# Kernel tuning notes

Hardware: AMD Instinct MI355X
Metric: run time of the kernel (lower is better)

## Reference

```python
import jax, jax.numpy as jnp
import numpy as np

N, E = 40000, 640000
IN_DIM, EDGE_DIM, HID = 128, 64, 128


def setup_inputs() -> dict:
    key = jax.random.key(0)
    ks = jax.random.split(key, 10)
    x = jax.random.normal(ks[0], (N, IN_DIM), dtype=jnp.float32)
    edge_index = jax.random.randint(ks[1], (2, E), 0, N, dtype=jnp.int64)
    edge_attr = jax.random.normal(ks[2], (E, EDGE_DIM), dtype=jnp.float32)
    # learned params (xavier-ish scaling)
    Wh_w = jax.random.normal(ks[3], (EDGE_DIM, HID), dtype=jnp.float32) / np.sqrt(EDGE_DIM)
    Wh_b = jnp.zeros((HID,), dtype=jnp.float32)
    Wn_w = jax.random.normal(ks[4], (2 * IN_DIM, HID), dtype=jnp.float32) / np.sqrt(2 * IN_DIM)
    Wn_b = jnp.zeros((HID,), dtype=jnp.float32)
    w_e = jax.random.normal(ks[5], (HID, 1), dtype=jnp.float32) / np.sqrt(HID)
    ft_w = jax.random.normal(ks[6], (IN_DIM, IN_DIM), dtype=jnp.float32) / np.sqrt(IN_DIM)
    ft_b = jnp.zeros((IN_DIM,), dtype=jnp.float32)
    return {"x": x, "edge_index": edge_index, "edge_attr": edge_attr,
            "Wh_w": Wh_w, "Wh_b": Wh_b, "Wn_w": Wn_w, "Wn_b": Wn_b,
            "w_e": w_e, "ft_w": ft_w, "ft_b": ft_b}


def reference(x, edge_index, edge_attr, Wh_w, Wh_b, Wn_w, Wn_b, w_e, ft_w, ft_b):
    src, dst = edge_index[0], edge_index[1]
    # gather endpoint features and run edge MLP: relu(W_h(e) + W_n([x_src; x_dst]))
    node_feat = jnp.concatenate([x[src], x[dst]], axis=1)          # [E, 2*in_dim]
    edge_h = edge_attr @ Wh_w + Wh_b                               # [E, hid]
    node_h = node_feat @ Wn_w + Wn_b                               # [E, hid]
    combined = jax.nn.relu(edge_h + node_h)
    scores = (combined @ w_e)[:, 0]                                # [E]
    alpha = jax.nn.softmax(scores, axis=0)                         # softmax over all edges
    # scatter-add weighted dst features into src nodes (same-type branch)
    local = jnp.zeros_like(x).at[src].add(-alpha[:, None] * x[dst])
    out = x + local
    out = out + out @ ft_w + ft_b
    return out
```

## Files before the change

### kernel.cpp

```cpp
#include <hip/hip_runtime.h>
#include <math.h>

#define N_NODES 40000
#define E_EDGES 640000
#define IN_DIM 128
#define EDGE_DIM 64
#define HID 128
#define EB 10000

typedef unsigned int u32;
typedef unsigned short u16;
typedef __attribute__((ext_vector_type(4))) float f32x4;
typedef __attribute__((ext_vector_type(8))) short bf16x8;

__device__ __forceinline__ float bf_lo(u32 d) { return __uint_as_float(d << 16); }
__device__ __forceinline__ float bf_hi(u32 d) { return __uint_as_float(d & 0xffff0000u); }
__device__ __forceinline__ u16 f2bf(float f) {
    u32 u = __float_as_uint(f);
    return (u16)((u + 0x7fffu + ((u >> 16) & 1u)) >> 16);
}


__global__ __launch_bounds__(256) void k_init(const float* __restrict__ x,
                                              u16* __restrict__ xb,
                                              u32* __restrict__ counts) {
    int i = blockIdx.x * 256 + threadIdx.x;
    xb[i] = f2bf(x[i]);
    if (i < N_NODES) counts[i] = 0;
}

__global__ __launch_bounds__(256) void k_trans(const float* __restrict__ Wh,
                                               u16* __restrict__ Whtb) {
    int i = blockIdx.x * 256 + threadIdx.x;
    int h = i >> 6;
    int k = i & 63;
    Whtb[i] = f2bf(Wh[k * HID + h]);
}

__global__ __launch_bounds__(256) void k_proj(const float* __restrict__ x,
                                              const float* __restrict__ Wn,
                                              const float* __restrict__ Whb,
                                              const float* __restrict__ Wnb,
                                              u16* __restrict__ P1b,
                                              u16* __restrict__ P2b) {
    __shared__ float xs[16][IN_DIM];
    const int rowBase = blockIdx.x * 16;

    const float4* xsrc = (const float4*)(x + (size_t)rowBase * IN_DIM);
    float4* xd = (float4*)&xs[0][0];
    for (int i = threadIdx.x; i < 16 * IN_DIM / 4; i += 256) xd[i] = xsrc[i];
    __syncthreads();

    const int h  = threadIdx.x & 127;
    const int rg = threadIdx.x >> 7;

    float acc1[8], acc2[8];
#pragma unroll
    for (int r = 0; r < 8; ++r) { acc1[r] = 0.f; acc2[r] = 0.f; }

    for (int k = 0; k < IN_DIM; ++k) {
        float wa = Wn[k * HID + h];
        float wb = Wn[(IN_DIM + k) * HID + h];
#pragma unroll
        for (int r = 0; r < 8; ++r) {
            float xv = xs[rg * 8 + r][k];
            acc1[r] += xv * wa;
            acc2[r] += xv * wb;
        }
    }
    const float bias = Whb[h] + Wnb[h];
#pragma unroll
    for (int r = 0; r < 8; ++r) {
        int row = rowBase + rg * 8 + r;
        P1b[(size_t)row * HID + h] = f2bf(acc1[r] + bias);
        P2b[(size_t)row * HID + h] = f2bf(acc2[r]);
    }
}

__global__ __launch_bounds__(256) void k_hist(const int* __restrict__ eidx,
                                              u32* __restrict__ counts) {
    int e = blockIdx.x * 256 + threadIdx.x;
    atomicAdd(&counts[eidx[e]], 1u);
}

__global__ __launch_bounds__(1024) void k_scan(const u32* __restrict__ counts,
                                               u32* __restrict__ off,
                                               u32* __restrict__ cur) {
    __shared__ u32 sums[1024];
    const int t = threadIdx.x;
    const int CH = 40;
    u32 local[CH];
    u32 s = 0;
    const int base = t * CH;
#pragma unroll
    for (int i = 0; i < CH; ++i) {
        int idx = base + i;
        u32 c = (idx < N_NODES) ? counts[idx] : 0u;
        local[i] = s;
        s += c;
    }
    sums[t] = s;
    __syncthreads();
    for (int o = 1; o < 1024; o <<= 1) {
        u32 v = (t >= o) ? sums[t - o] : 0u;
        __syncthreads();
        sums[t] += v;
        __syncthreads();
    }
    const u32 pre = sums[t] - s;
#pragma unroll
    for (int i = 0; i < CH; ++i) {
        int idx = base + i;
        if (idx < N_NODES) {
            u32 v = pre + local[i];
            off[idx] = v;
            cur[idx] = v;
        }
    }
    if (t == 1023) off[N_NODES] = sums[1023];
}

__global__ __launch_bounds__(256) void k_edge(const int* __restrict__ eidx,
                                              const float* __restrict__ ea,
                                              const u16* __restrict__ Whtb,
                                              const u16* __restrict__ P1b,
                                              const u16* __restrict__ P2b,
                                              const float* __restrict__ we,
                                              float* __restrict__ expS,
                                              float* __restrict__ partials) {
    __shared__ float Ps[64][132];
    __shared__ float wsumLds[4];
    const int e0 = blockIdx.x * 64;
    const int t = threadIdx.x;

    {
        const int m = t >> 2, c4 = t & 3;
        int src = eidx[e0 + m];
        int dst = eidx[E_EDGES + e0 + m];
        const uint4* p1 = (const uint4*)(P1b + (size_t)src * HID + c4 * 32);
        const uint4* p2 = (const uint4*)(P2b + (size_t)dst * HID + c4 * 32);
#pragma unroll
        for (int i = 0; i < 4; ++i) {
            uint4 ua = p1[i], ub = p2[i];
            u32 da[4] = {ua.x, ua.y, ua.z, ua.w};
            u32 db[4] = {ub.x, ub.y, ub.z, ub.w};
#pragma unroll
            for (int j = 0; j < 4; ++j) {
                Ps[m][c4 * 32 + i * 8 + 2 * j]     = bf_lo(da[j]) + bf_lo(db[j]);
                Ps[m][c4 * 32 + i * 8 + 2 * j + 1] = bf_hi(da[j]) + bf_hi(db[j]);
            }
        }
    }
    __syncthreads();

    const int w = t >> 6, lane = t & 63;
    const int mrow = lane & 15, quad = lane >> 4;
    const int mt = w;

    const float* arow = ea + (size_t)(e0 + mt * 16 + mrow) * EDGE_DIM + quad * 8;
    bf16x8 a0, a1;
#pragma unroll
    for (int ks = 0; ks < 2; ++ks) {
        float4 f0 = *(const float4*)(arow + ks * 32);
        float4 f1 = *(const float4*)(arow + ks * 32 + 4);
        bf16x8& af = ks ? a1 : a0;
        af[0] = (short)f2bf(f0.x); af[1] = (short)f2bf(f0.y);
        af[2] = (short)f2bf(f0.z); af[3] = (short)f2bf(f0.w);
        af[4] = (short)f2bf(f1.x); af[5] = (short)f2bf(f1.y);
        af[6] = (short)f2bf(f1.z); af[7] = (short)f2bf(f1.w);
    }

    float wsum[4] = {0.f, 0.f, 0.f, 0.f};
    const u16* bbase = Whtb + (size_t)mrow * EDGE_DIM + quad * 8;
#pragma unroll
    for (int nt = 0; nt < 8; ++nt) {
        const u16* bp = bbase + nt * 16 * EDGE_DIM;
        bf16x8 b0 = *(const bf16x8*)(bp);
        bf16x8 b1 = *(const bf16x8*)(bp + 32);
        f32x4 c = {0.f, 0.f, 0.f, 0.f};
        c = __builtin_amdgcn_mfma_f32_16x16x32_bf16(a0, b0, c, 0, 0, 0);
        c = __builtin_amdgcn_mfma_f32_16x16x32_bf16(a1, b1, c, 0, 0, 0);
        float wv = we[nt * 16 + mrow];
#pragma unroll
        for (int r = 0; r < 4; ++r) {
            float v = c[r] + Ps[mt * 16 + quad * 4 + r][nt * 16 + mrow];
            wsum[r] += fmaxf(v, 0.f) * wv;
        }
    }

#pragma unroll
    for (int off = 1; off < 16; off <<= 1) {
#pragma unroll
        for (int r = 0; r < 4; ++r) wsum[r] += __shfl_xor(wsum[r], off, 16);
    }
    float ex[4]; float s4 = 0.f;
#pragma unroll
    for (int r = 0; r < 4; ++r) { ex[r] = __expf(wsum[r]); s4 += ex[r]; }
    if (mrow == 0) {
#pragma unroll
        for (int r = 0; r < 4; ++r) expS[e0 + mt * 16 + quad * 4 + r] = ex[r];
    }
    s4 += __shfl_xor(s4, 16, 64);
    s4 += __shfl_xor(s4, 32, 64);
    if (lane == 0) wsumLds[w] = s4;
    __syncthreads();
    if (t == 0) partials[blockIdx.x] = wsumLds[0] + wsumLds[1] + wsumLds[2] + wsumLds[3];
}

__global__ __launch_bounds__(256) void k_sum(const float* __restrict__ partials,
                                             float* __restrict__ sumExp) {
    float s = 0.f;
    for (int i = threadIdx.x; i < EB; i += 256) s += partials[i];
#pragma unroll
    for (int off = 1; off < 64; off <<= 1) s += __shfl_xor(s, off, 64);
    __shared__ float ws4[4];
    if ((threadIdx.x & 63) == 0) ws4[threadIdx.x >> 6] = s;
    __syncthreads();
    if (threadIdx.x == 0) sumExp[0] = ws4[0] + ws4[1] + ws4[2] + ws4[3];
}

__global__ __launch_bounds__(256) void k_fill(const int* __restrict__ eidx,
                                              const float* __restrict__ expS,
                                              const float* __restrict__ sumExp,
                                              u32* __restrict__ cur,
                                              u32* __restrict__ sdst,
                                              float* __restrict__ sa) {
    const float invS = 1.0f / sumExp[0];
    int e = blockIdx.x * 256 + threadIdx.x;
    int src = eidx[e];
    int dst = eidx[E_EDGES + e];
    u32 pos = atomicAdd(&cur[src], 1u);
    sdst[pos] = (u32)dst;
    sa[pos]   = -expS[e] * invS;
}

__global__ __launch_bounds__(256) void k_accum(const u32* __restrict__ off,
                                               const u32* __restrict__ sdst,
                                               const float* __restrict__ sa,
                                               const u16* __restrict__ xb,
                                               float* __restrict__ out) {
    const int lane = threadIdx.x & 63;
    const int n = blockIdx.x * 4 + (threadIdx.x >> 6);
    const u32 o0 = off[n], o1 = off[n + 1];

    float acc0 = 0.f, acc1 = 0.f;
    for (u32 base = o0; base < o1; base += 64) {
        u32 j = base + (u32)lane;
        u32 dv = 0; float av = 0.f;
        if (j < o1) { dv = sdst[j]; av = sa[j]; }
        int cnt = (int)min(64u, o1 - base);
        for (int jj = 0; jj < cnt; ++jj) {
            u32 dst = __shfl(dv, jj, 64);
            float a = __shfl(av, jj, 64);
            u32 d = ((const u32*)(xb + (size_t)dst * IN_DIM))[lane];
            acc0 = fmaf(a, bf_lo(d), acc0);
            acc1 = fmaf(a, bf_hi(d), acc1);
        }
    }
    float* op = out + (size_t)n * IN_DIM + 2 * lane;
    op[0] = acc0;
    op[1] = acc1;
}

__global__ __launch_bounds__(256) void k_final(const float* __restrict__ x,
                                               const float* __restrict__ ft,
                                               const float* __restrict__ ftb,
                                               float* __restrict__ out) {
    __shared__ float ys[16][IN_DIM];
    const int rowBase = blockIdx.x * 16;

    const float4* xsrc = (const float4*)(x + (size_t)rowBase * IN_DIM);
    const float4* lsrc = (const float4*)(out + (size_t)rowBase * IN_DIM);
    float4* yd = (float4*)&ys[0][0];
    for (int i = threadIdx.x; i < 16 * IN_DIM / 4; i += 256) {
        float4 a = xsrc[i];
        float4 b = lsrc[i];
        a.x += b.x; a.y += b.y; a.z += b.z; a.w += b.w;
        yd[i] = a;
    }
    __syncthreads();

    const int h  = threadIdx.x & 127;
    const int rg = threadIdx.x >> 7;

    float acc[8];
#pragma unroll
    for (int r = 0; r < 8; ++r) acc[r] = 0.f;

    for (int k = 0; k < IN_DIM; ++k) {
        float w = ft[k * IN_DIM + h];
#pragma unroll
        for (int r = 0; r < 8; ++r) acc[r] += ys[rg * 8 + r][k] * w;
    }
    const float b = ftb[h];
#pragma unroll
    for (int r = 0; r < 8; ++r) {
        int row = rowBase + rg * 8 + r;
        out[(size_t)row * IN_DIM + h] = ys[rg * 8 + r][h] + acc[r] + b;
    }
}

extern "C" void kernel_launch(void* const* d_in, const int* in_sizes, int n_in,
                              void* d_out, int out_size, void* d_ws, size_t ws_size,
                              hipStream_t stream) {
    const float* x    = (const float*)d_in[0];
    const int*   eidx = (const int*)d_in[1];
    const float* ea   = (const float*)d_in[2];
    const float* Whw  = (const float*)d_in[3];
    const float* Whb  = (const float*)d_in[4];
    const float* Wnw  = (const float*)d_in[5];
    const float* Wnb  = (const float*)d_in[6];
    const float* we   = (const float*)d_in[7];
    const float* ftw  = (const float*)d_in[8];
    const float* ftb  = (const float*)d_in[9];
    float* out = (float*)d_out;

    u16*   P1b      = (u16*)d_ws;
    u16*   P2b      = P1b + (size_t)N_NODES * HID;
    u16*   xb       = P2b + (size_t)N_NODES * HID;
    u16*   Whtb     = xb + (size_t)N_NODES * IN_DIM;
    float* expS     = (float*)(Whtb + (size_t)EDGE_DIM * HID);
    float* partials = expS + (size_t)E_EDGES;
    float* sumExp   = partials + EB;
    u32*   counts   = (u32*)(sumExp + 1);
    u32*   off      = counts + N_NODES;
    u32*   cur      = off + N_NODES + 1;
    u32*   sdst     = cur + N_NODES;
    float* sa       = (float*)(sdst + E_EDGES);

    k_init <<<(N_NODES * IN_DIM) / 256, 256, 0, stream>>>(x, xb, counts);
    k_trans<<<(EDGE_DIM * HID) / 256, 256, 0, stream>>>(Whw, Whtb);
    k_proj <<<N_NODES / 16, 256, 0, stream>>>(x, Wnw, Whb, Wnb, P1b, P2b);
    k_hist <<<E_EDGES / 256, 256, 0, stream>>>(eidx, counts);
    k_scan <<<1, 1024, 0, stream>>>(counts, off, cur);
    k_edge <<<EB, 256, 0, stream>>>(eidx, ea, Whtb, P1b, P2b, we, expS, partials);
    k_sum  <<<1, 256, 0, stream>>>(partials, sumExp);
    k_fill <<<E_EDGES / 256, 256, 0, stream>>>(eidx, expS, sumExp, cur, sdst, sa);
    k_accum<<<N_NODES / 4, 256, 0, stream>>>(off, sdst, sa, xb, out);
    k_final<<<N_NODES / 16, 256, 0, stream>>>(x, ftw, ftb, out);
}
```

Baseline: 587.4 us.

## Move node projection and final transform GEMMs onto bf16 MFMA

```diff
diff --git a/kernel.cpp b/kernel.cpp
--- a/kernel.cpp
+++ b/kernel.cpp
@@ -19,6 +19,9 @@
     u32 u = __float_as_uint(f);
     return (u16)((u + 0x7fffu + ((u >> 16) & 1u)) >> 16);
 }
+__device__ __forceinline__ u32 pack_bf(float lo, float hi) {
+    return ((u32)f2bf(hi) << 16) | (u32)f2bf(lo);
+}
 
 
 __global__ __launch_bounds__(256) void k_init(const float* __restrict__ x,
@@ -29,51 +32,63 @@
     if (i < N_NODES) counts[i] = 0;
 }
 
-__global__ __launch_bounds__(256) void k_trans(const float* __restrict__ Wh,
-                                               u16* __restrict__ Whtb) {
+__global__ __launch_bounds__(256) void k_trans(const float* __restrict__ Whw,
+                                               const float* __restrict__ Wnw,
+                                               const float* __restrict__ ftw,
+                                               u16* __restrict__ Whtb,
+                                               u16* __restrict__ WnAT,
+                                               u16* __restrict__ WnBT,
+                                               u16* __restrict__ fttb) {
     int i = blockIdx.x * 256 + threadIdx.x;
-    int h = i >> 6;
-    int k = i & 63;
-    Whtb[i] = f2bf(Wh[k * HID + h]);
-}
-
-__global__ __launch_bounds__(256) void k_proj(const float* __restrict__ x,
-                                              const float* __restrict__ Wn,
+    if (i < 8192) {
+        int h = i >> 6, k = i & 63;
+        Whtb[i] = f2bf(Whw[k * HID + h]);
+    } else if (i < 24576) {
+        int j = i - 8192, h = j >> 7, k = j & 127;
+        WnAT[j] = f2bf(Wnw[k * HID + h]);
+    } else if (i < 40960) {
+        int j = i - 24576, h = j >> 7, k = j & 127;
+        WnBT[j] = f2bf(Wnw[(IN_DIM + k) * HID + h]);
+    } else {
+        int j = i - 40960, h = j >> 7, k = j & 127;
+        fttb[j] = f2bf(ftw[k * IN_DIM + h]);
+    }
+}
+
+__global__ __launch_bounds__(256) void k_proj(const u16* __restrict__ xb,
+                                              const u16* __restrict__ WnAT,
+                                              const u16* __restrict__ WnBT,
                                               const float* __restrict__ Whb,
                                               const float* __restrict__ Wnb,
                                               u16* __restrict__ P1b,
                                               u16* __restrict__ P2b) {
-    __shared__ float xs[16][IN_DIM];
-    const int rowBase = blockIdx.x * 16;
-
-    const float4* xsrc = (const float4*)(x + (size_t)rowBase * IN_DIM);
-    float4* xd = (float4*)&xs[0][0];
-    for (int i = threadIdx.x; i < 16 * IN_DIM / 4; i += 256) xd[i] = xsrc[i];
-    __syncthreads();
-
-    const int h  = threadIdx.x & 127;
-    const int rg = threadIdx.x >> 7;
-
-    float acc1[8], acc2[8];
-#pragma unroll
-    for (int r = 0; r < 8; ++r) { acc1[r] = 0.f; acc2[r] = 0.f; }
-
-    for (int k = 0; k < IN_DIM; ++k) {
-        float wa = Wn[k * HID + h];
-        float wb = Wn[(IN_DIM + k) * HID + h];
-#pragma unroll
-        for (int r = 0; r < 8; ++r) {
-            float xv = xs[rg * 8 + r][k];
-            acc1[r] += xv * wa;
-            acc2[r] += xv * wb;
-        }
-    }
-    const float bias = Whb[h] + Wnb[h];
-#pragma unroll
-    for (int r = 0; r < 8; ++r) {
-        int row = rowBase + rg * 8 + r;
-        P1b[(size_t)row * HID + h] = f2bf(acc1[r] + bias);
-        P2b[(size_t)row * HID + h] = f2bf(acc2[r]);
+    const int t = threadIdx.x, w = t >> 6, lane = t & 63;
+    const int mrow = lane & 15, quad = lane >> 4;
+    const int rowBase = blockIdx.x * 64 + w * 16;
+
+    bf16x8 a[4];
+    const u16* ar = xb + (size_t)(rowBase + mrow) * IN_DIM + quad * 8;
+#pragma unroll
+    for (int ks = 0; ks < 4; ++ks) a[ks] = *(const bf16x8*)(ar + ks * 32);
+
+#pragma unroll
+    for (int nt = 0; nt < 8; ++nt) {
+        const u16* b1p = WnAT + (size_t)(nt * 16 + mrow) * IN_DIM + quad * 8;
+        const u16* b2p = WnBT + (size_t)(nt * 16 + mrow) * IN_DIM + quad * 8;
+        f32x4 c1 = {0.f, 0.f, 0.f, 0.f}, c2 = {0.f, 0.f, 0.f, 0.f};
+#pragma unroll
+        for (int ks = 0; ks < 4; ++ks) {
+            c1 = __builtin_amdgcn_mfma_f32_16x16x32_bf16(a[ks], *(const bf16x8*)(b1p + ks * 32), c1, 0, 0, 0);
+            c2 = __builtin_amdgcn_mfma_f32_16x16x32_bf16(a[ks], *(const bf16x8*)(b2p + ks * 32), c2, 0, 0, 0);
+        }
+        const int col = nt * 16 + mrow;
+        const float bias = Whb[col] + Wnb[col];
+#pragma unroll
+        for (int r = 0; r < 4; ++r) {
+            int row = rowBase + quad * 4 + r;
+            P1b[(size_t)row * HID + col] = f2bf(c1[r] + bias);
+            P2b[(size_t)row * HID + col] = f2bf(c2[r]);
+        }
     }
 }
 
@@ -128,7 +143,7 @@
                                               const float* __restrict__ we,
                                               float* __restrict__ expS,
                                               float* __restrict__ partials) {
-    __shared__ float Ps[64][132];
+    __shared__ u32 Psp[64][68];
     __shared__ float wsumLds[4];
     const int e0 = blockIdx.x * 64;
     const int t = threadIdx.x;
@@ -144,11 +159,12 @@
             uint4 ua = p1[i], ub = p2[i];
             u32 da[4] = {ua.x, ua.y, ua.z, ua.w};
             u32 db[4] = {ub.x, ub.y, ub.z, ub.w};
-#pragma unroll
-            for (int j = 0; j < 4; ++j) {
-                Ps[m][c4 * 32 + i * 8 + 2 * j]     = bf_lo(da[j]) + bf_lo(db[j]);
-                Ps[m][c4 * 32 + i * 8 + 2 * j + 1] = bf_hi(da[j]) + bf_hi(db[j]);
-            }
+            uint4 o;
+            o.x = pack_bf(bf_lo(da[0]) + bf_lo(db[0]), bf_hi(da[0]) + bf_hi(db[0]));
+            o.y = pack_bf(bf_lo(da[1]) + bf_lo(db[1]), bf_hi(da[1]) + bf_hi(db[1]));
+            o.z = pack_bf(bf_lo(da[2]) + bf_lo(db[2]), bf_hi(da[2]) + bf_hi(db[2]));
+            o.w = pack_bf(bf_lo(da[3]) + bf_lo(db[3]), bf_hi(da[3]) + bf_hi(db[3]));
+            *(uint4*)&Psp[m][c4 * 16 + i * 4] = o;
         }
     }
     __syncthreads();
@@ -183,8 +199,9 @@
         float wv = we[nt * 16 + mrow];
 #pragma unroll
         for (int r = 0; r < 4; ++r) {
-            float v = c[r] + Ps[mt * 16 + quad * 4 + r][nt * 16 + mrow];
-            wsum[r] += fmaxf(v, 0.f) * wv;
+            u32 u = Psp[mt * 16 + quad * 4 + r][nt * 8 + (mrow >> 1)];
+            float p = (mrow & 1) ? bf_hi(u) : bf_lo(u);
+            wsum[r] += fmaxf(c[r] + p, 0.f) * wv;
         }
     }
 
@@ -263,40 +280,56 @@
 }
 
 __global__ __launch_bounds__(256) void k_final(const float* __restrict__ x,
-                                               const float* __restrict__ ft,
+                                               const u16* __restrict__ fttb,
                                                const float* __restrict__ ftb,
                                                float* __restrict__ out) {
-    __shared__ float ys[16][IN_DIM];
-    const int rowBase = blockIdx.x * 16;
-
-    const float4* xsrc = (const float4*)(x + (size_t)rowBase * IN_DIM);
-    const float4* lsrc = (const float4*)(out + (size_t)rowBase * IN_DIM);
-    float4* yd = (float4*)&ys[0][0];
-    for (int i = threadIdx.x; i < 16 * IN_DIM / 4; i += 256) {
-        float4 a = xsrc[i];
-        float4 b = lsrc[i];
-        a.x += b.x; a.y += b.y; a.z += b.z; a.w += b.w;
-        yd[i] = a;
-    }
-    __syncthreads();
-
-    const int h  = threadIdx.x & 127;
-    const int rg = threadIdx.x >> 7;
-
-    float acc[8];
-#pragma unroll
-    for (int r = 0; r < 8; ++r) acc[r] = 0.f;
-
-    for (int k = 0; k < IN_DIM; ++k) {
-        float w = ft[k * IN_DIM + h];
-#pragma unroll
-        for (int r = 0; r < 8; ++r) acc[r] += ys[rg * 8 + r][k] * w;
-    }
-    const float b = ftb[h];
-#pragma unroll
-    for (int r = 0; r < 8; ++r) {
-        int row = rowBase + rg * 8 + r;
-        out[(size_t)row * IN_DIM + h] = ys[rg * 8 + r][h] + acc[r] + b;
+    __shared__ u32 ybp[64][68];
+    const int t = threadIdx.x;
+    const int rb = blockIdx.x * 64;
+
+    {
+        const int rr = t >> 2, seg = t & 3;
+        const float4* xp = (const float4*)(x + (size_t)(rb + rr) * IN_DIM + seg * 32);
+        const float4* lp = (const float4*)(out + (size_t)(rb + rr) * IN_DIM + seg * 32);
+#pragma unroll
+        for (int i = 0; i < 4; ++i) {
+            float4 xa = xp[2 * i], xc = xp[2 * i + 1];
+            float4 la = lp[2 * i], lc = lp[2 * i + 1];
+            uint4 o;
+            o.x = pack_bf(xa.x + la.x, xa.y + la.y);
+            o.y = pack_bf(xa.z + la.z, xa.w + la.w);
+            o.z = pack_bf(xc.x + lc.x, xc.y + lc.y);
+            o.w = pack_bf(xc.z + lc.z, xc.w + lc.w);
+            *(uint4*)&ybp[rr][seg * 16 + i * 4] = o;
+        }
+    }
+    __syncthreads();
+
+    const int w = t >> 6, lane = t & 63;
+    const int mrow = lane & 15, quad = lane >> 4;
+    const int rowBase = rb + w * 16;
+
+    bf16x8 a[4];
+#pragma unroll
+    for (int ks = 0; ks < 4; ++ks)
+        a[ks] = *(const bf16x8*)&ybp[w * 16 + mrow][ks * 16 + quad * 4];
+
+#pragma unroll
+    for (int nt = 0; nt < 8; ++nt) {
+        const u16* bp = fttb + (size_t)(nt * 16 + mrow) * IN_DIM + quad * 8;
+        f32x4 c = {0.f, 0.f, 0.f, 0.f};
+#pragma unroll
+        for (int ks = 0; ks < 4; ++ks)
+            c = __builtin_amdgcn_mfma_f32_16x16x32_bf16(a[ks], *(const bf16x8*)(bp + ks * 32), c, 0, 0, 0);
+        const int col = nt * 16 + mrow;
+        const float fb = ftb[col];
+#pragma unroll
+        for (int r = 0; r < 4; ++r) {
+            int row = rowBase + quad * 4 + r;
+            size_t idx = (size_t)row * IN_DIM + col;
+            float y = x[idx] + out[idx];
+            out[idx] = y + c[r] + fb;
+        }
     }
 }
 
@@ -319,7 +352,10 @@
     u16*   P2b      = P1b + (size_t)N_NODES * HID;
     u16*   xb       = P2b + (size_t)N_NODES * HID;
     u16*   Whtb     = xb + (size_t)N_NODES * IN_DIM;
-    float* expS     = (float*)(Whtb + (size_t)EDGE_DIM * HID);
+    u16*   WnAT     = Whtb + (size_t)EDGE_DIM * HID;
+    u16*   WnBT     = WnAT + (size_t)HID * IN_DIM;
+    u16*   fttb     = WnBT + (size_t)HID * IN_DIM;
+    float* expS     = (float*)(fttb + (size_t)IN_DIM * IN_DIM);
     float* partials = expS + (size_t)E_EDGES;
     float* sumExp   = partials + EB;
     u32*   counts   = (u32*)(sumExp + 1);
@@ -329,13 +365,13 @@
     float* sa       = (float*)(sdst + E_EDGES);
 
     k_init <<<(N_NODES * IN_DIM) / 256, 256, 0, stream>>>(x, xb, counts);
-    k_trans<<<(EDGE_DIM * HID) / 256, 256, 0, stream>>>(Whw, Whtb);
-    k_proj <<<N_NODES / 16, 256, 0, stream>>>(x, Wnw, Whb, Wnb, P1b, P2b);
+    k_trans<<<224, 256, 0, stream>>>(Whw, Wnw, ftw, Whtb, WnAT, WnBT, fttb);
+    k_proj <<<N_NODES / 64, 256, 0, stream>>>(xb, WnAT, WnBT, Whb, Wnb, P1b, P2b);
     k_hist <<<E_EDGES / 256, 256, 0, stream>>>(eidx, counts);
     k_scan <<<1, 1024, 0, stream>>>(counts, off, cur);
     k_edge <<<EB, 256, 0, stream>>>(eidx, ea, Whtb, P1b, P2b, we, expS, partials);
     k_sum  <<<1, 256, 0, stream>>>(partials, sumExp);
     k_fill <<<E_EDGES / 256, 256, 0, stream>>>(eidx, expS, sumExp, cur, sdst, sa);
     k_accum<<<N_NODES / 4, 256, 0, stream>>>(off, sdst, sa, xb, out);
-    k_final<<<N_NODES / 16, 256, 0, stream>>>(x, ftw, ftb, out);
-}
+    k_final<<<N_NODES / 64, 256, 0, stream>>>(x, fttb, ftb, out);
+}
```

Measured after the change: 570.3 us. -2.9%, faster.
